# Kernel tuning notes

Hardware: AMD Instinct MI355X
Metric: run time of the kernel (lower is better)

## Reference

```python
import jax, jax.numpy as jnp
import numpy as np

B, L, S, T, C = 8192, 16, 256, 1000, 500  # trees, leaves/tree, hidden, tables, columns
EPS = 1e-5  # torch LayerNorm default eps


def layer_norm(x, g, b):
    mu = x.mean(-1, keepdims=True)
    var = ((x - mu) ** 2).mean(-1, keepdims=True)
    return (x - mu) * jax.lax.rsqrt(var + EPS) * g + b


def setup_inputs() -> dict:
    key = jax.random.key(0)
    ks = jax.random.split(key, 16)
    s5 = 5 * S

    def lin(k, fan_in, shape):
        bound = 1.0 / np.sqrt(fan_in)
        return jax.random.uniform(k, shape, jnp.float32, -bound, bound)

    return {
        "leaf_ids": jax.random.randint(ks[0], (B, L), 0, T),
        "action_ids": jax.random.randint(ks[1], (B,), 0, T),
        # multi-hot join-condition vectors (original scatters 1s by column index)
        "join_cols": (jax.random.uniform(ks[2], (B, L - 1, C)) < 0.01).astype(jnp.float32),
        "emb": jax.random.normal(ks[3], (T, S), jnp.float32),
        "ln_g": jnp.ones((S,), jnp.float32),
        "ln_b": jnp.zeros((S,), jnp.float32),
        "jc_W": lin(ks[4], C, (C, S)), "jc_b": lin(ks[5], C, (S,)),
        "W1": lin(ks[6], S, (S, s5)), "b1": lin(ks[7], S, (s5,)),
        "W2": lin(ks[8], S, (S, s5)), "b2": lin(ks[9], S, (s5,)),
        "W0": lin(ks[10], S, (S, s5)), "b0": lin(ks[11], S, (s5,)),
        "fc_W": lin(ks[12], 2 * S, (2 * S, S)), "fc_b": lin(ks[13], 2 * S, (S,)),
        "out_W": lin(ks[14], S, (S, 1)), "out_b": lin(ks[15], S, (1,)),
    }


def reference(leaf_ids, action_ids, join_cols, emb, ln_g, ln_b, jc_W, jc_b,
              W1, b1, W2, b2, W0, b0, fc_W, fc_b, out_W, out_b):
    # Leaves: h = LayerNorm(embedding(table_id)), c = 0
    h = layer_norm(emb[leaf_ids], ln_g, ln_b)        # [B, L, S]
    c = jnp.zeros_like(h)
    # Bottom-up level sweep over complete binary trees (log2(L) = 4 levels)
    off, n = 0, L // 2
    while n >= 1:
        hl, hr = h[:, 0::2], h[:, 1::2]               # [B, n, S]
        cl, cr = c[:, 0::2], c[:, 1::2]
        inputx = join_cols[:, off:off + n] @ jc_W + jc_b
        z = hl @ W1 + b1 + hr @ W2 + b2 + inputx @ W0 + b0  # [B, n, 5S]
        a, i, f1, f2, o = jnp.split(z, 5, axis=-1)
        c = jnp.tanh(a) * jax.nn.sigmoid(i) + jax.nn.sigmoid(f1) * cl + jax.nn.sigmoid(f2) * cr
        h = jax.nn.sigmoid(o) * jnp.tanh(c)
        off += n
        n //= 2
    state_h = h[:, 0]                                 # [B, S] root encodings
    action_h = layer_norm(emb[action_ids], ln_g, ln_b)  # [B, S] action leaf encodings
    x = jnp.concatenate([state_h, action_h], axis=-1)   # [B, 2S]
    return jax.nn.relu(x @ fc_W + fc_b) @ out_W + out_b  # [B, 1]
```

## Files before the change

### kernel.cpp

```cpp
#include <hip/hip_runtime.h>
#include <hip/hip_bf16.h>
#include <stdint.h>

#define NB 8192
#define NL 16
#define NS 256
#define NT 1000
#define NC 500
#define NS5 1280
#define NROWS_JC (NB*15)

typedef __attribute__((ext_vector_type(8))) short bf16x8;
typedef __attribute__((ext_vector_type(4))) float f32x4;

typedef __attribute__((address_space(1))) const void gas_void;
typedef __attribute__((address_space(3))) void las_void;

__device__ __forceinline__ void g2l16(const void* g, void* l) {
  __builtin_amdgcn_global_load_lds((gas_void*)g, (las_void*)l, 16, 0, 0);
}

__device__ __forceinline__ float sigf(float x) { return 1.f / (1.f + __expf(-x)); }
__device__ __forceinline__ float tanhfast(float x) {
  float e = __expf(2.f * fabsf(x));
  float t = 1.f - 2.f / (e + 1.f);
  return copysignf(t, x);
}
__device__ __forceinline__ unsigned short bf16b(float x) {
  __hip_bfloat16 h = __float2bfloat16(x);
  return *reinterpret_cast<unsigned short*>(&h);
}
__device__ __forceinline__ float b2f(unsigned short v) {
  union { unsigned u; float f; } x;
  x.u = (unsigned)v << 16;
  return x.f;
}

__device__ __forceinline__ int origcol(int slice, int nc) {
  int q = nc / 80, rem = nc % 80;
  int g = rem / 16, u16 = rem % 16;
  int U = slice * 64 + q * 16 + u16;
  return g * 256 + U;
}

#define PB_INPUTX (NROWS_JC / 8)
#define PB_LN     (PB_INPUTX + NT)
#define PB_W12    (PB_LN + 480)
#define PB_FCW    (PB_W12 + 64)
#define PB_TOTAL  (PB_FCW + 5)

__global__ __launch_bounds__(256) void prologue_kernel(
    const float* __restrict__ jc, const float* __restrict__ jcW,
    const float* __restrict__ jcb, unsigned short* __restrict__ inpx,
    const float* __restrict__ emb, const float* __restrict__ lng,
    const float* __restrict__ lnb, unsigned short* __restrict__ ob16,
    const float* __restrict__ W1, const float* __restrict__ W2,
    const float* __restrict__ W0, unsigned short* __restrict__ w12p,
    const float* __restrict__ fcW, unsigned short* __restrict__ fcwp,
    const float* __restrict__ b1, const float* __restrict__ b2,
    const float* __restrict__ b0, float* __restrict__ bias_zp) {
  __shared__ float rs[4], rs2[4];
  const int bid = blockIdx.x;
  const int tid = threadIdx.x;

  if (bid < PB_INPUTX) {
    int wv = tid >> 6, lane = tid & 63;
    size_t row0 = (size_t)bid * 8 + wv * 2;
    const float* jr0 = jc + row0 * NC;
    const float* jr1 = jc + (row0 + 1) * NC;
    float4 p0 = *(const float4*)(jr0 + lane * 4);
    float4 q0 = *(const float4*)(jr1 + lane * 4);
    float4 p1 = make_float4(0.f, 0.f, 0.f, 0.f);
    float4 q1 = make_float4(0.f, 0.f, 0.f, 0.f);
    if (lane < 61) {
      p1 = *(const float4*)(jr0 + 256 + lane * 4);
      q1 = *(const float4*)(jr1 + 256 + lane * 4);
    }
    const float4 jb = *(const float4*)(jcb + lane * 4);
    float a0 = jb.x, a1 = jb.y, a2 = jb.z, a3 = jb.w;
    float c0 = jb.x, c1 = jb.y, c2 = jb.z, c3 = jb.w;

#define GATHER_MASK(val, cbase, d0, d1, d2, d3)                       \
    {                                                                 \
      unsigned long long m = __ballot((val) != 0.f);                  \
      while (m) {                                                     \
        int l = __ffsll(m) - 1;                                       \
        m &= m - 1;                                                   \
        int c = (cbase) + l * 4;                                      \
        const float4 w = *(const float4*)(jcW + (size_t)c * NS + lane * 4); \
        d0 += w.x; d1 += w.y; d2 += w.z; d3 += w.w;                   \
      }                                                               \
    }
    GATHER_MASK(p0.x, 0, a0, a1, a2, a3) GATHER_MASK(p0.y, 1, a0, a1, a2, a3)
    GATHER_MASK(p0.z, 2, a0, a1, a2, a3) GATHER_MASK(p0.w, 3, a0, a1, a2, a3)
    GATHER_MASK(p1.x, 256, a0, a1, a2, a3) GATHER_MASK(p1.y, 257, a0, a1, a2, a3)
    GATHER_MASK(p1.z, 258, a0, a1, a2, a3) GATHER_MASK(p1.w, 259, a0, a1, a2, a3)
    GATHER_MASK(q0.x, 0, c0, c1, c2, c3) GATHER_MASK(q0.y, 1, c0, c1, c2, c3)
    GATHER_MASK(q0.z, 2, c0, c1, c2, c3) GATHER_MASK(q0.w, 3, c0, c1, c2, c3)
    GATHER_MASK(q1.x, 256, c0, c1, c2, c3) GATHER_MASK(q1.y, 257, c0, c1, c2, c3)
    GATHER_MASK(q1.z, 258, c0, c1, c2, c3) GATHER_MASK(q1.w, 259, c0, c1, c2, c3)
#undef GATHER_MASK

    ushort4 o;
    o.x = bf16b(a0); o.y = bf16b(a1); o.z = bf16b(a2); o.w = bf16b(a3);
    *(ushort4*)(inpx + row0 * NS + lane * 4) = o;
    o.x = bf16b(c0); o.y = bf16b(c1); o.z = bf16b(c2); o.w = bf16b(c3);
    *(ushort4*)(inpx + (row0 + 1) * NS + lane * 4) = o;
  } else if (bid < PB_LN) {
    int t = bid - PB_INPUTX;
    int i = tid;
    int lane = i & 63, wv = i >> 6;
    float x = emb[t * NS + i];
    float s = x, s2 = x * x;
    for (int o = 1; o < 64; o <<= 1) {
      s += __shfl_xor(s, o);
      s2 += __shfl_xor(s2, o);
    }
    if (lane == 0) { rs[wv] = s; rs2[wv] = s2; }
    __syncthreads();
    float S = rs[0] + rs[1] + rs[2] + rs[3];
    float S2 = rs2[0] + rs2[1] + rs2[2] + rs2[3];
    float mu = S * (1.f / NS);
    float var = S2 * (1.f / NS) - mu * mu;
    float y = (x - mu) * rsqrtf(var + 1e-5f) * lng[i] + lnb[i];
    ob16[t * NS + i] = bf16b(y);
  } else if (bid < PB_W12) {
    int e = (bid - PB_LN) * 256 + tid;
    int kg = e & 3;
    int r = e >> 2;
    int nc = r % 320; r /= 320;
    int kc = r % 24;
    int slice = r / 24;
    int oc = origcol(slice, nc);
    int kbase = kc * 32 + kg * 8;
    unsigned short tmp[8];
#pragma unroll
    for (int j = 0; j < 8; ++j) {
      int k = kbase + j;
      float x;
      if (k < 256) x = W1[(size_t)k * NS5 + oc];
      else if (k < 512) x = W2[(size_t)(k - 256) * NS5 + oc];
      else x = W0[(size_t)(k - 512) * NS5 + oc];
      tmp[j] = bf16b(x);
    }
    ushort4 v0 = make_ushort4(tmp[0], tmp[1], tmp[2], tmp[3]);
    ushort4 v1 = make_ushort4(tmp[4], tmp[5], tmp[6], tmp[7]);
    size_t dst = (size_t)(slice * 24 + kc) * 20480 + (size_t)nc * 64 + kg * 16;
    *(ushort4*)((char*)w12p + dst) = v0;
    *(ushort4*)((char*)w12p + dst + 8) = v1;
  } else if (bid < PB_FCW) {
    int e = (bid - PB_W12) * 256 + tid;
    int kg = e & 3;
    int r = e >> 2;
    int nc = r & 255;
    int kc = r >> 8;
    int kbase = kc * 32 + kg * 8;
    unsigned short tmp[8];
#pragma unroll
    for (int j = 0; j < 8; ++j) tmp[j] = bf16b(fcW[(size_t)(kbase + j) * NS + nc]);
    ushort4 v0 = make_ushort4(tmp[0], tmp[1], tmp[2], tmp[3]);
    ushort4 v1 = make_ushort4(tmp[4], tmp[5], tmp[6], tmp[7]);
    size_t dst = (size_t)kc * 16384 + (size_t)nc * 64 + kg * 16;
    *(ushort4*)((char*)fcwp + dst) = v0;
    *(ushort4*)((char*)fcwp + dst + 8) = v1;
  } else {
    int pc = (bid - PB_FCW) * 256 + tid;
    if (pc < NS5) {
      int slice = pc / 320, nc = pc % 320;
      int oc = origcol(slice, nc);
      bias_zp[pc] = b1[oc] + b2[oc] + b0[oc];
    }
  }
}

template <bool FIRST, bool LAST>
__global__ __launch_bounds__(256, 2) void level_kernel(
    const unsigned short* __restrict__ h_in,
    const unsigned* __restrict__ c_in,
    const unsigned short* __restrict__ inpx,
    const unsigned short* __restrict__ w12p,
    const float* __restrict__ bias_zp,
    unsigned short* __restrict__ h_out,
    unsigned* __restrict__ c_out,
    unsigned short* __restrict__ state_out,
    const int* __restrict__ leaf,
    int log2n, int joff) {
  __shared__ __align__(1024) char ldsA[2 * 16384];
  const int tid = threadIdx.x, lane = tid & 63, wv = tid >> 6;
  const int m0 = blockIdx.x * 128;
  const int slice = blockIdx.y;
  const int n = 1 << log2n;

  f32x4 acc[8][5];
#pragma unroll
  for (int a = 0; a < 8; ++a)
#pragma unroll
    for (int t = 0; t < 5; ++t) acc[a][t] = (f32x4){0.f, 0.f, 0.f, 0.f};

  const int rl64 = wv * 16 + (lane >> 2);
  const int ss = (lane & 3) ^ ((rl64 >> 1) & 3);
  const int mlo = m0 + rl64, mhi = mlo + 64;
  const char* h0lo; const char* h1lo; const char* h0hi; const char* h1hi;
  if (FIRST) {
    h0lo = (const char*)h_in + ((size_t)leaf[2 * mlo] * 512 + (size_t)ss * 16);
    h1lo = (const char*)h_in + ((size_t)leaf[2 * mlo + 1] * 512 + (size_t)ss * 16);
    h0hi = (const char*)h_in + ((size_t)leaf[2 * mhi] * 512 + (size_t)ss * 16);
    h1hi = (const char*)h_in + ((size_t)leaf[2 * mhi + 1] * 512 + (size_t)ss * 16);
  } else {
    h0lo = (const char*)h_in + ((size_t)mlo * 1024 + (size_t)ss * 16);
    h1lo = h0lo;
    h0hi = (const char*)h_in + ((size_t)mhi * 1024 + (size_t)ss * 16);
    h1hi = h0hi;
  }
  const char* xlo = (const char*)inpx +
      (((size_t)(mlo >> log2n) * 15 + joff + (mlo & (n - 1))) * 512 + (size_t)ss * 16);
  const char* xhi = (const char*)inpx +
      (((size_t)(mhi >> log2n) * 15 + joff + (mhi & (n - 1))) * 512 + (size_t)ss * 16);
  char* adst = ldsA + wv * 1024;

  auto srcA = [&](int kc, int j) -> const char* {
    const char* h0 = j ? h0hi : h0lo;
    const char* h1 = j ? h1hi : h1lo;
    const char* xs = j ? xhi : xlo;
    if (FIRST) {
      return (kc < 8) ? h0 + kc * 64
           : (kc < 16) ? h1 + (kc - 8) * 64
                       : xs + (kc - 16) * 64;
    }
    return (kc < 16) ? h0 + kc * 64 : xs + (kc - 16) * 64;
  };
  auto stageA = [&](int kt, int buf) {
    char* db = adst + buf * 16384;
    g2l16(srcA(2 * kt, 0), db);
    g2l16(srcA(2 * kt, 1), db + 4096);
    g2l16(srcA(2 * kt + 1, 0), db + 8192);
    g2l16(srcA(2 * kt + 1, 1), db + 12288);
  };

  const int aoff = (lane & 15) * 64 + (((lane >> 4) ^ ((lane >> 1) & 3)) << 4);
  const char* gB = (const char*)w12p + (size_t)slice * 24 * 20480 +
                   (size_t)(wv * 80 + (lane & 15)) * 64 + (size_t)(lane >> 4) * 16;

  bf16x8 bcur[5], bnxt[5];
  auto loadB = [&](int kc, bf16x8* dst) {
    const char* gk = gB + (size_t)kc * 20480;
#pragma unroll
    for (int g = 0; g < 5; ++g) dst[g] = *(const bf16x8*)(gk + g * 1024);
  };

#define CLUSTER(pA, bset)                                                           \
  {                                                                                 \
    bf16x8 a0 = *(const bf16x8*)(pA);                                               \
    bf16x8 a1 = *(const bf16x8*)((pA) + 1024);                                      \
    bf16x8 a2 = *(const bf16x8*)((pA) + 2048);                                      \
    bf16x8 a3 = *(const bf16x8*)((pA) + 3072);                                      \
    bf16x8 a4 = *(const bf16x8*)((pA) + 4096);                                      \
    bf16x8 a5 = *(const bf16x8*)((pA) + 5120);                                      \
    bf16x8 a6 = *(const bf16x8*)((pA) + 6144);                                      \
    bf16x8 a7 = *(const bf16x8*)((pA) + 7168);                                      \
    _Pragma("unroll")                                                               \
    for (int g = 0; g < 5; ++g) {                                                   \
      acc[0][g] = __builtin_amdgcn_mfma_f32_16x16x32_bf16(a0, bset[g], acc[0][g], 0, 0, 0); \
      acc[1][g] = __builtin_amdgcn_mfma_f32_16x16x32_bf16(a1, bset[g], acc[1][g], 0, 0, 0); \
      acc[2][g] = __builtin_amdgcn_mfma_f32_16x16x32_bf16(a2, bset[g], acc[2][g], 0, 0, 0); \
      acc[3][g] = __builtin_amdgcn_mfma_f32_16x16x32_bf16(a3, bset[g], acc[3][g], 0, 0, 0); \
      acc[4][g] = __builtin_amdgcn_mfma_f32_16x16x32_bf16(a4, bset[g], acc[4][g], 0, 0, 0); \
      acc[5][g] = __builtin_amdgcn_mfma_f32_16x16x32_bf16(a5, bset[g], acc[5][g], 0, 0, 0); \
      acc[6][g] = __builtin_amdgcn_mfma_f32_16x16x32_bf16(a6, bset[g], acc[6][g], 0, 0, 0); \
      acc[7][g] = __builtin_amdgcn_mfma_f32_16x16x32_bf16(a7, bset[g], acc[7][g], 0, 0, 0); \
    }                                                                               \
  }

  stageA(0, 0);
  loadB(0, bcur);
  asm volatile("s_waitcnt vmcnt(0)" ::: "memory");
  __builtin_amdgcn_s_barrier();

  for (int kt = 0; kt < 12; ++kt) {
    const int buf = kt & 1;
    stageA(kt < 11 ? kt + 1 : 11, buf ^ 1);
    __builtin_amdgcn_sched_barrier(0);
    loadB(2 * kt + 1, bnxt);
    const char* pA = ldsA + buf * 16384 + aoff;
    CLUSTER(pA, bcur);
    loadB(2 * kt + 2 < 24 ? 2 * kt + 2 : 0, bcur);
    CLUSTER(pA + 8192, bnxt);
    __builtin_amdgcn_sched_barrier(0);
    asm volatile("s_waitcnt vmcnt(5)" ::: "memory");
    __builtin_amdgcn_sched_barrier(0);
    __builtin_amdgcn_s_barrier();
  }
#undef CLUSTER

  float bias[5];
#pragma unroll
  for (int g = 0; g < 5; ++g)
    bias[g] = bias_zp[slice * 320 + wv * 80 + g * 16 + (lane & 15)];
  const int u = slice * 64 + wv * 16 + (lane & 15);

#pragma unroll
  for (int rt = 0; rt < 8; ++rt) {
    const int base = m0 + rt * 16 + (lane >> 4) * 4;
    float hv[4], cv[4];
#pragma unroll
    for (int r = 0; r < 4; ++r) {
      int row = base + r;
      float za = acc[rt][0][r] + bias[0];
      float zi = acc[rt][1][r] + bias[1];
      float zo = acc[rt][4][r] + bias[4];
      float cnew = tanhfast(za) * sigf(zi);
      if (!FIRST) {
        float zf1 = acc[rt][2][r] + bias[2];
        float zf2 = acc[rt][3][r] + bias[3];
        unsigned pc = c_in[(size_t)row * NS + u];
        float cl = b2f((unsigned short)(pc & 0xffff));
        float cr = b2f((unsigned short)(pc >> 16));
        cnew += sigf(zf1) * cl + sigf(zf2) * cr;
      }
      cv[r] = cnew;
      hv[r] = sigf(zo) * tanhfast(cnew);
    }
    if (LAST) {
#pragma unroll
      for (int r = 0; r < 4; ++r)
        state_out[(size_t)(base + r) * NS + u] = bf16b(hv[r]);
    } else {
#pragma unroll
      for (int r = 0; r < 4; ++r)
        h_out[(size_t)(base + r) * NS + u] = bf16b(hv[r]);
      const size_t pb = (size_t)(base >> 1) * NS + u;
      c_out[pb] = (unsigned)bf16b(cv[0]) | ((unsigned)bf16b(cv[1]) << 16);
      c_out[pb + NS] = (unsigned)bf16b(cv[2]) | ((unsigned)bf16b(cv[3]) << 16);
    }
  }
}

__global__ __launch_bounds__(256, 2) void fc_mfma(
    const unsigned short* __restrict__ stateb,
    const unsigned short* __restrict__ ln_b16,
    const int* __restrict__ action_ids, const unsigned short* __restrict__ fcwp,
    const float* __restrict__ fcb, const float* __restrict__ outW,
    const float* __restrict__ outb, float* __restrict__ out) {
  __shared__ __align__(1024) char ldsA[2 * 8192];
  __shared__ float red[64][4];
  const int tid = threadIdx.x, lane = tid & 63, wv = tid >> 6;
  const int m0 = blockIdx.x * 64;

  f32x4 acc[4][4];
#pragma unroll
  for (int a = 0; a < 4; ++a)
#pragma unroll
    for (int t = 0; t < 4; ++t) acc[a][t] = (f32x4){0.f, 0.f, 0.f, 0.f};

  const int rl = wv * 16 + (lane >> 2);
  const int ss = (lane & 3) ^ ((rl >> 1) & 3);
  const int m = m0 + rl;
  const char* src0 = (const char*)stateb + ((size_t)m * 512 + (size_t)ss * 16);
  const char* src1 =
      (const char*)ln_b16 + ((size_t)action_ids[m] * 512 + (size_t)ss * 16);
  char* adst = ldsA + wv * 1024;

  auto srcA = [&](int kc) -> const char* {
    return (kc < 8) ? src0 + kc * 64 : src1 + (kc - 8) * 64;
  };
  auto stageA = [&](int kt, int buf) {
    g2l16(srcA(2 * kt), adst + buf * 8192);
    g2l16(srcA(2 * kt + 1), adst + buf * 8192 + 4096);
  };

  const int aoff = (lane & 15) * 64 + (((lane >> 4) ^ ((lane >> 1) & 3)) << 4);
  const char* gB = (const char*)fcwp +
                   (size_t)(wv * 64 + (lane & 15)) * 64 + (size_t)(lane >> 4) * 16;

  bf16x8 bcur[4], bnxt[4];
  auto loadB = [&](int kc, bf16x8* dst) {
    const char* gk = gB + (size_t)kc * 16384;
#pragma unroll
    for (int t = 0; t < 4; ++t) dst[t] = *(const bf16x8*)(gk + t * 1024);
  };

  stageA(0, 0);
  loadB(0, bcur);
  asm volatile("s_waitcnt vmcnt(0)" ::: "memory");
  __builtin_amdgcn_s_barrier();

  for (int kt = 0; kt < 8; ++kt) {
    const int buf = kt & 1;
    stageA(kt < 7 ? kt + 1 : 7, buf ^ 1);
    __builtin_amdgcn_sched_barrier(0);
    loadB(2 * kt + 1, bnxt);
    const char* pA = ldsA + buf * 8192 + aoff;
    bf16x8 a0 = *(const bf16x8*)(pA);
    bf16x8 a1 = *(const bf16x8*)(pA + 1024);
    bf16x8 a2 = *(const bf16x8*)(pA + 2048);
    bf16x8 a3 = *(const bf16x8*)(pA + 3072);
#pragma unroll
    for (int t = 0; t < 4; ++t) {
      acc[0][t] = __builtin_amdgcn_mfma_f32_16x16x32_bf16(a0, bcur[t], acc[0][t], 0, 0, 0);
      acc[1][t] = __builtin_amdgcn_mfma_f32_16x16x32_bf16(a1, bcur[t], acc[1][t], 0, 0, 0);
      acc[2][t] = __builtin_amdgcn_mfma_f32_16x16x32_bf16(a2, bcur[t], acc[2][t], 0, 0, 0);
      acc[3][t] = __builtin_amdgcn_mfma_f32_16x16x32_bf16(a3, bcur[t], acc[3][t], 0, 0, 0);
    }
    loadB(2 * kt + 2 < 16 ? 2 * kt + 2 : 0, bcur);
    bf16x8 c0 = *(const bf16x8*)(pA + 4096);
    bf16x8 c1 = *(const bf16x8*)(pA + 5120);
    bf16x8 c2 = *(const bf16x8*)(pA + 6144);
    bf16x8 c3 = *(const bf16x8*)(pA + 7168);
#pragma unroll
    for (int t = 0; t < 4; ++t) {
      acc[0][t] = __builtin_amdgcn_mfma_f32_16x16x32_bf16(c0, bnxt[t], acc[0][t], 0, 0, 0);
      acc[1][t] = __builtin_amdgcn_mfma_f32_16x16x32_bf16(c1, bnxt[t], acc[1][t], 0, 0, 0);
      acc[2][t] = __builtin_amdgcn_mfma_f32_16x16x32_bf16(c2, bnxt[t], acc[2][t], 0, 0, 0);
      acc[3][t] = __builtin_amdgcn_mfma_f32_16x16x32_bf16(c3, bnxt[t], acc[3][t], 0, 0, 0);
    }
    __builtin_amdgcn_sched_barrier(0);
    asm volatile("s_waitcnt vmcnt(4)" ::: "memory");
    __builtin_amdgcn_sched_barrier(0);
    __builtin_amdgcn_s_barrier();
  }

  float fb[4], ow[4];
#pragma unroll
  for (int t = 0; t < 4; ++t) {
    int col = wv * 64 + t * 16 + (lane & 15);
    fb[t] = fcb[col];
    ow[t] = outW[col];
  }
#pragma unroll
  for (int rt = 0; rt < 4; ++rt) {
#pragma unroll
    for (int r = 0; r < 4; ++r) {
      float s = 0.f;
#pragma unroll
      for (int t = 0; t < 4; ++t)
        s += fmaxf(acc[rt][t][r] + fb[t], 0.f) * ow[t];
      s += __shfl_xor(s, 1);
      s += __shfl_xor(s, 2);
      s += __shfl_xor(s, 4);
      s += __shfl_xor(s, 8);
      if ((lane & 15) == 0) red[rt * 16 + (lane >> 4) * 4 + r][wv] = s;
    }
  }
  __syncthreads();
  if (tid < 64)
    out[m0 + tid] = red[tid][0] + red[tid][1] + red[tid][2] + red[tid][3] + outb[0];
}

extern "C" void kernel_launch(void* const* d_in, const int* in_sizes, int n_in,
                              void* d_out, int out_size, void* d_ws, size_t ws_size,
                              hipStream_t stream) {
  const int* leaf_ids = (const int*)d_in[0];
  const int* action_ids = (const int*)d_in[1];
  const float* join_cols = (const float*)d_in[2];
  const float* emb = (const float*)d_in[3];
  const float* ln_g = (const float*)d_in[4];
  const float* ln_b = (const float*)d_in[5];
  const float* jc_W = (const float*)d_in[6];
  const float* jc_b = (const float*)d_in[7];
  const float* W1 = (const float*)d_in[8];
  const float* b1 = (const float*)d_in[9];
  const float* W2 = (const float*)d_in[10];
  const float* b2 = (const float*)d_in[11];
  const float* W0 = (const float*)d_in[12];
  const float* b0 = (const float*)d_in[13];
  const float* fc_W = (const float*)d_in[14];
  const float* fc_b = (const float*)d_in[15];
  const float* out_W = (const float*)d_in[16];
  const float* out_b = (const float*)d_in[17];

  char* ws = (char*)d_ws;
  size_t o = 0;
  auto alloc = [&](size_t bytes) {
    size_t r = o;
    o += (bytes + 255) & ~(size_t)255;
    return r;
  };
  unsigned short* ln_b16 = (unsigned short*)(ws + alloc((size_t)NT * NS * 2));
  unsigned short* w12p = (unsigned short*)(ws + alloc((size_t)4 * 24 * 20480));
  unsigned short* fcwp = (unsigned short*)(ws + alloc((size_t)16 * 16384));
  float* bias_zp = (float*)(ws + alloc((size_t)NS5 * 4));
  unsigned short* inpx = (unsigned short*)(ws + alloc((size_t)NROWS_JC * NS * 2));
  unsigned short* hX = (unsigned short*)(ws + alloc((size_t)NB * 8 * NS * 2));
  unsigned short* hY = (unsigned short*)(ws + alloc((size_t)NB * 4 * NS * 2));
  unsigned* cX = (unsigned*)(ws + alloc((size_t)NB * 8 * NS * 2));
  unsigned* cY = (unsigned*)(ws + alloc((size_t)NB * 4 * NS * 2));
  unsigned short* stateb = (unsigned short*)(ws + alloc((size_t)NB * NS * 2));
  (void)ws_size; (void)in_sizes; (void)n_in; (void)out_size;

  prologue_kernel<<<PB_TOTAL, 256, 0, stream>>>(
      join_cols, jc_W, jc_b, inpx, emb, ln_g, ln_b, ln_b16, W1, W2, W0, w12p,
      fc_W, fcwp, b1, b2, b0, bias_zp);

  level_kernel<true, false><<<dim3(512, 4), 256, 0, stream>>>(
      ln_b16, nullptr, inpx, w12p, bias_zp, hX, cX, nullptr, leaf_ids, 3, 0);
  level_kernel<false, false><<<dim3(256, 4), 256, 0, stream>>>(
      hX, cX, inpx, w12p, bias_zp, hY, cY, nullptr, leaf_ids, 2, 8);
  level_kernel<false, false><<<dim3(128, 4), 256, 0, stream>>>(
      hY, cY, inpx, w12p, bias_zp, hX, cX, nullptr, leaf_ids, 1, 12);
  level_kernel<false, true><<<dim3(64, 4), 256, 0, stream>>>(
      hX, cX, inpx, w12p, bias_zp, nullptr, nullptr, stateb, leaf_ids, 0, 14);

  fc_mfma<<<NB / 64, 256, 0, stream>>>(stateb, ln_b16, action_ids, fcwp, fc_b,
                                       out_W, out_b, (float*)d_out);
}
```

Baseline: 332.8 us.

## Specialize first tree level to skip forget gates since leaf cell state is zero

Adds a dedicated level-0 kernel that computes only the a, i and o gate columns, because the leaf cell state is zero and the forget-gate terms vanish. The prologue packs a reduced 768-column weight and bias layout for this kernel. The new kernel uses 64-row tiles, three N-fragments per wave and higher occupancy. This reduces matrix work on the largest level, at the cost of extra prologue packing and a separate kernel to maintain.

```diff
diff --git a/kernel.cpp b/kernel.cpp
--- a/kernel.cpp
+++ b/kernel.cpp
@@ -42,12 +42,20 @@
   int U = slice * 64 + q * 16 + u16;
   return g * 256 + U;
 }
+__device__ __forceinline__ int origcol3(int slice, int nc) {
+  int q = nc / 48, rem = nc % 48;
+  int g = rem / 16, u16 = rem % 16;
+  int U = slice * 64 + q * 16 + u16;
+  const int G[3] = {0, 1, 4};
+  return G[g] * 256 + U;
+}
 
 #define PB_INPUTX (NROWS_JC / 8)
 #define PB_LN     (PB_INPUTX + NT)
 #define PB_W12    (PB_LN + 480)
-#define PB_FCW    (PB_W12 + 64)
-#define PB_TOTAL  (PB_FCW + 5)
+#define PB_W12L0  (PB_W12 + 288)
+#define PB_FCW    (PB_W12L0 + 64)
+#define PB_TOTAL  (PB_FCW + 8)
 
 __global__ __launch_bounds__(256) void prologue_kernel(
     const float* __restrict__ jc, const float* __restrict__ jcW,
@@ -56,9 +64,11 @@
     const float* __restrict__ lnb, unsigned short* __restrict__ ob16,
     const float* __restrict__ W1, const float* __restrict__ W2,
     const float* __restrict__ W0, unsigned short* __restrict__ w12p,
+    unsigned short* __restrict__ w12p0,
     const float* __restrict__ fcW, unsigned short* __restrict__ fcwp,
     const float* __restrict__ b1, const float* __restrict__ b2,
-    const float* __restrict__ b0, float* __restrict__ bias_zp) {
+    const float* __restrict__ b0, float* __restrict__ bias_zp,
+    float* __restrict__ bias_zp3) {
   __shared__ float rs[4], rs2[4];
   const int bid = blockIdx.x;
   const int tid = threadIdx.x;
@@ -148,8 +158,32 @@
     size_t dst = (size_t)(slice * 24 + kc) * 20480 + (size_t)nc * 64 + kg * 16;
     *(ushort4*)((char*)w12p + dst) = v0;
     *(ushort4*)((char*)w12p + dst + 8) = v1;
+  } else if (bid < PB_W12L0) {
+    int e = (bid - PB_W12) * 256 + tid;
+    int kg = e & 3;
+    int r = e >> 2;
+    int nc = r % 192; r /= 192;
+    int kc = r % 24;
+    int slice = r / 24;
+    int oc = origcol3(slice, nc);
+    int kbase = kc * 32 + kg * 8;
+    unsigned short tmp[8];
+#pragma unroll
+    for (int j = 0; j < 8; ++j) {
+      int k = kbase + j;
+      float x;
+      if (k < 256) x = W1[(size_t)k * NS5 + oc];
+      else if (k < 512) x = W2[(size_t)(k - 256) * NS5 + oc];
+      else x = W0[(size_t)(k - 512) * NS5 + oc];
+      tmp[j] = bf16b(x);
+    }
+    ushort4 v0 = make_ushort4(tmp[0], tmp[1], tmp[2], tmp[3]);
+    ushort4 v1 = make_ushort4(tmp[4], tmp[5], tmp[6], tmp[7]);
+    size_t dst = (size_t)(slice * 24 + kc) * 12288 + (size_t)nc * 64 + kg * 16;
+    *(ushort4*)((char*)w12p0 + dst) = v0;
+    *(ushort4*)((char*)w12p0 + dst + 8) = v1;
   } else if (bid < PB_FCW) {
-    int e = (bid - PB_W12) * 256 + tid;
+    int e = (bid - PB_W12L0) * 256 + tid;
     int kg = e & 3;
     int r = e >> 2;
     int nc = r & 255;
@@ -163,13 +197,134 @@
     size_t dst = (size_t)kc * 16384 + (size_t)nc * 64 + kg * 16;
     *(ushort4*)((char*)fcwp + dst) = v0;
     *(ushort4*)((char*)fcwp + dst + 8) = v1;
-  } else {
+  } else if (bid < PB_FCW + 5) {
     int pc = (bid - PB_FCW) * 256 + tid;
     if (pc < NS5) {
       int slice = pc / 320, nc = pc % 320;
       int oc = origcol(slice, nc);
       bias_zp[pc] = b1[oc] + b2[oc] + b0[oc];
     }
+  } else {
+    int pc = (bid - PB_FCW - 5) * 256 + tid;
+    if (pc < 768) {
+      int slice = pc / 192, nc = pc % 192;
+      int oc = origcol3(slice, nc);
+      bias_zp3[pc] = b1[oc] + b2[oc] + b0[oc];
+    }
+  }
+}
+
+__global__ __launch_bounds__(256, 4) void level0_kernel(
+    const unsigned short* __restrict__ h_in,
+    const unsigned short* __restrict__ inpx,
+    const unsigned short* __restrict__ w12p0,
+    const float* __restrict__ bias_zp3,
+    unsigned short* __restrict__ h_out,
+    unsigned* __restrict__ c_out,
+    const int* __restrict__ leaf) {
+  __shared__ __align__(1024) char ldsA[2 * 8192];
+  const int tid = threadIdx.x, lane = tid & 63, wv = tid >> 6;
+  const int m0 = blockIdx.x * 64;
+  const int slice = blockIdx.y;
+
+  f32x4 acc[4][3];
+#pragma unroll
+  for (int a = 0; a < 4; ++a)
+#pragma unroll
+    for (int t = 0; t < 3; ++t) acc[a][t] = (f32x4){0.f, 0.f, 0.f, 0.f};
+
+  const int rl = wv * 16 + (lane >> 2);
+  const int ss = (lane & 3) ^ ((rl >> 1) & 3);
+  const int m = m0 + rl;
+  const char* hsrc0 = (const char*)h_in + ((size_t)leaf[2 * m] * 512 + (size_t)ss * 16);
+  const char* hsrc1 = (const char*)h_in + ((size_t)leaf[2 * m + 1] * 512 + (size_t)ss * 16);
+  const char* xsrc = (const char*)inpx +
+      (((size_t)(m >> 3) * 15 + (m & 7)) * 512 + (size_t)ss * 16);
+  char* adst = ldsA + wv * 1024;
+
+  auto srcA = [&](int kc) -> const char* {
+    return (kc < 8) ? hsrc0 + kc * 64
+         : (kc < 16) ? hsrc1 + (kc - 8) * 64
+                     : xsrc + (kc - 16) * 64;
+  };
+  auto stageA = [&](int kt, int buf) {
+    g2l16(srcA(2 * kt), adst + buf * 8192);
+    g2l16(srcA(2 * kt + 1), adst + buf * 8192 + 4096);
+  };
+
+  const int aoff = (lane & 15) * 64 + (((lane >> 4) ^ ((lane >> 1) & 3)) << 4);
+  const char* gB = (const char*)w12p0 + (size_t)slice * 24 * 12288 +
+                   (size_t)(wv * 48 + (lane & 15)) * 64 + (size_t)(lane >> 4) * 16;
+
+  bf16x8 bcur[3], bnxt[3];
+  auto loadB = [&](int kc, bf16x8* dst) {
+    const char* gk = gB + (size_t)kc * 12288;
+    dst[0] = *(const bf16x8*)(gk);
+    dst[1] = *(const bf16x8*)(gk + 1024);
+    dst[2] = *(const bf16x8*)(gk + 2048);
+  };
+
+#define CLUSTER0(pA, bset)                                                          \
+  {                                                                                 \
+    bf16x8 a0 = *(const bf16x8*)(pA);                                               \
+    bf16x8 a1 = *(const bf16x8*)((pA) + 1024);                                      \
+    bf16x8 a2 = *(const bf16x8*)((pA) + 2048);                                      \
+    bf16x8 a3 = *(const bf16x8*)((pA) + 3072);                                      \
+    _Pragma("unroll")                                                               \
+    for (int g = 0; g < 3; ++g) {                                                   \
+      acc[0][g] = __builtin_amdgcn_mfma_f32_16x16x32_bf16(a0, bset[g], acc[0][g], 0, 0, 0); \
+      acc[1][g] = __builtin_amdgcn_mfma_f32_16x16x32_bf16(a1, bset[g], acc[1][g], 0, 0, 0); \
+      acc[2][g] = __builtin_amdgcn_mfma_f32_16x16x32_bf16(a2, bset[g], acc[2][g], 0, 0, 0); \
+      acc[3][g] = __builtin_amdgcn_mfma_f32_16x16x32_bf16(a3, bset[g], acc[3][g], 0, 0, 0); \
+    }                                                                               \
+  }
+
+  stageA(0, 0);
+  loadB(0, bcur);
+  asm volatile("s_waitcnt vmcnt(0)" ::: "memory");
+  __builtin_amdgcn_s_barrier();
+
+  for (int kt = 0; kt < 12; ++kt) {
+    const int buf = kt & 1;
+    stageA(kt < 11 ? kt + 1 : 11, buf ^ 1);
+    __builtin_amdgcn_sched_barrier(0);
+    loadB(2 * kt + 1, bnxt);
+    const char* pA = ldsA + buf * 8192 + aoff;
+    CLUSTER0(pA, bcur);
+    loadB(2 * kt + 2 < 24 ? 2 * kt + 2 : 0, bcur);
+    CLUSTER0(pA + 4096, bnxt);
+    __builtin_amdgcn_sched_barrier(0);
+    asm volatile("s_waitcnt vmcnt(3)" ::: "memory");
+    __builtin_amdgcn_sched_barrier(0);
+    __builtin_amdgcn_s_barrier();
+  }
+#undef CLUSTER0
+
+  float bias[3];
+#pragma unroll
+  for (int g = 0; g < 3; ++g)
+    bias[g] = bias_zp3[slice * 192 + wv * 48 + g * 16 + (lane & 15)];
+  const int u = slice * 64 + wv * 16 + (lane & 15);
+
+#pragma unroll
+  for (int rt = 0; rt < 4; ++rt) {
+    const int base = m0 + rt * 16 + (lane >> 4) * 4;
+    float hv[4], cv[4];
+#pragma unroll
+    for (int r = 0; r < 4; ++r) {
+      float za = acc[rt][0][r] + bias[0];
+      float zi = acc[rt][1][r] + bias[1];
+      float zo = acc[rt][2][r] + bias[2];
+      float cnew = tanhfast(za) * sigf(zi);
+      cv[r] = cnew;
+      hv[r] = sigf(zo) * tanhfast(cnew);
+    }
+#pragma unroll
+    for (int r = 0; r < 4; ++r)
+      h_out[(size_t)(base + r) * NS + u] = bf16b(hv[r]);
+    const size_t pb = (size_t)(base >> 1) * NS + u;
+    c_out[pb] = (unsigned)bf16b(cv[0]) | ((unsigned)bf16b(cv[1]) << 16);
+    c_out[pb + NS] = (unsigned)bf16b(cv[2]) | ((unsigned)bf16b(cv[3]) << 16);
   }
 }
 
@@ -477,8 +632,10 @@
   };
   unsigned short* ln_b16 = (unsigned short*)(ws + alloc((size_t)NT * NS * 2));
   unsigned short* w12p = (unsigned short*)(ws + alloc((size_t)4 * 24 * 20480));
+  unsigned short* w12p0 = (unsigned short*)(ws + alloc((size_t)4 * 24 * 12288));
   unsigned short* fcwp = (unsigned short*)(ws + alloc((size_t)16 * 16384));
   float* bias_zp = (float*)(ws + alloc((size_t)NS5 * 4));
+  float* bias_zp3 = (float*)(ws + alloc((size_t)768 * 4));
   unsigned short* inpx = (unsigned short*)(ws + alloc((size_t)NROWS_JC * NS * 2));
   unsigned short* hX = (unsigned short*)(ws + alloc((size_t)NB * 8 * NS * 2));
   unsigned short* hY = (unsigned short*)(ws + alloc((size_t)NB * 4 * NS * 2));
@@ -489,10 +646,10 @@
 
   prologue_kernel<<<PB_TOTAL, 256, 0, stream>>>(
       join_cols, jc_W, jc_b, inpx, emb, ln_g, ln_b, ln_b16, W1, W2, W0, w12p,
-      fc_W, fcwp, b1, b2, b0, bias_zp);
-
-  level_kernel<true, false><<<dim3(512, 4), 256, 0, stream>>>(
-      ln_b16, nullptr, inpx, w12p, bias_zp, hX, cX, nullptr, leaf_ids, 3, 0);
+      w12p0, fc_W, fcwp, b1, b2, b0, bias_zp, bias_zp3);
+
+  level0_kernel<<<dim3(1024, 4), 256, 0, stream>>>(
+      ln_b16, inpx, w12p0, bias_zp3, hX, cX, leaf_ids);
   level_kernel<false, false><<<dim3(256, 4), 256, 0, stream>>>(
       hX, cX, inpx, w12p, bias_zp, hY, cY, nullptr, leaf_ids, 2, 8);
   level_kernel<false, false><<<dim3(128, 4), 256, 0, stream>>>(
```

Result: slower. 346.8 us (+4.2%).
